# Kernel optimization log

Hardware: AMD Instinct MI355X
Metric: run time of the kernel (lower is better)

## Reference

```python
import jax, jax.numpy as jnp
import numpy as np
from jax import lax

DIM = 192
HEADS = 8
HID = int(DIM * 4.0)

def setup_inputs() -> dict:
    key = jax.random.key(0)
    ks = jax.random.split(key, 10)
    b, c, h, w = 4, DIM, 256, DIM  # w must equal dim for the Mlp over last axis
    x = jax.random.normal(ks[0], (b, c, h, w), dtype=jnp.float32)
    return {
        "x": x,
        "ln1_w": jnp.ones((DIM,), jnp.float32),
        "ln1_b": jnp.zeros((DIM,), jnp.float32),
        "temperature": jnp.ones((HEADS, 1, 1), jnp.float32),
        "qkv_w": jax.random.normal(ks[1], (3 * DIM, DIM), jnp.float32) * 0.02,
        "dw_w": jax.random.normal(ks[2], (3 * DIM, 1, 3, 3), jnp.float32) * 0.1,
        "proj_w": jax.random.normal(ks[3], (DIM, DIM), jnp.float32) * 0.02,
        "ln2_w": jnp.ones((DIM,), jnp.float32),
        "ln2_b": jnp.zeros((DIM,), jnp.float32),
        "fc1_w": jax.random.normal(ks[4], (HID, DIM), jnp.float32) * 0.02,
        "fc1_b": jnp.zeros((HID,), jnp.float32),
        "fc2_w": jax.random.normal(ks[5], (DIM, HID), jnp.float32) * 0.02,
        "fc2_b": jnp.zeros((DIM,), jnp.float32),
    }

def _layernorm_chan(x, w, b):
    # WithBias LayerNorm over the channel axis, per spatial location (to_3d -> LN -> to_4d)
    mu = jnp.mean(x, axis=1, keepdims=True)
    var = jnp.mean((x - mu) ** 2, axis=1, keepdims=True)
    y = (x - mu) / jnp.sqrt(var + 1e-5)
    return y * w[None, :, None, None] + b[None, :, None, None]

def _l2norm(x, axis=-1, eps=1e-12):
    n = jnp.sqrt(jnp.sum(x * x, axis=axis, keepdims=True))
    return x / jnp.maximum(n, eps)

def _attention(x, temperature, qkv_w, dw_w, proj_w):
    b, c, h, w = x.shape
    # 1x1 conv (pointwise GEMM) then 3x3 depthwise conv
    qkv = jnp.einsum('oc,bchw->bohw', qkv_w, x)
    qkv = lax.conv_general_dilated(qkv, dw_w, window_strides=(1, 1), padding='SAME',
                                   feature_group_count=3 * c,
                                   dimension_numbers=('NCHW', 'OIHW', 'NCHW'))
    q, k, v = jnp.split(qkv, 3, axis=1)
    ch = c // HEADS
    q = q.reshape(b, HEADS, ch, h * w)
    k = k.reshape(b, HEADS, ch, h * w)
    v = v.reshape(b, HEADS, ch, h * w)
    q = _l2norm(q)
    k = _l2norm(k)
    attn = jnp.einsum('bhcn,bhdn->bhcd', q, k) * temperature  # [b,H,ch,ch] channel attention
    attn = jax.nn.softmax(attn, axis=-1)
    out = jnp.einsum('bhcd,bhdn->bhcn', attn, v).reshape(b, c, h, w)
    return jnp.einsum('oc,bchw->bohw', proj_w, out)

def _mlp(x, fc1_w, fc1_b, fc2_w, fc2_b):
    # nn.Linear applied on the LAST axis (w == dim), matching the original quirk
    h1 = jnp.einsum('bchw,ow->bcho', x, fc1_w) + fc1_b
    h1 = jax.nn.gelu(h1, approximate=False)
    return jnp.einsum('bcho,do->bchd', h1, fc2_w) + fc2_b

def reference(x, ln1_w, ln1_b, temperature, qkv_w, dw_w, proj_w, ln2_w, ln2_b, fc1_w, fc1_b, fc2_w, fc2_b):
    x = x + _attention(_layernorm_chan(x, ln1_w, ln1_b), temperature, qkv_w, dw_w, proj_w)
    x = x + _mlp(_layernorm_chan(x, ln2_w, ln2_b), fc1_w, fc1_b, fc2_w, fc2_b)
    return x
```

## Files before the change

### kernel.cpp

```cpp
#include <hip/hip_runtime.h>
#include <math.h>

#define SSP   49152
#define HDIM  256
#define WDIM  192
#define CDIM  192
#define NHEAD 8
#define CH    24
#define OC3   576
#define HIDF  768
#define NB    4
#define SCCH  24

typedef short bf16x8 __attribute__((ext_vector_type(8)));
typedef short bf16x4 __attribute__((ext_vector_type(4)));
typedef float f32x4  __attribute__((ext_vector_type(4)));

__device__ inline short f2bf(float f) {
  unsigned u = __float_as_uint(f);
  u += 0x7fffu + ((u >> 16) & 1u);
  return (short)(u >> 16);
}
__device__ inline float bf2f(short h) {
  return __uint_as_float(((unsigned)(unsigned short)h) << 16);
}

__device__ inline void gl_lds16(const short* g, short* l) {
  __builtin_amdgcn_global_load_lds(
      (const __attribute__((address_space(1))) unsigned int*)g,
      (__attribute__((address_space(3))) unsigned int*)l, 16, 0, 0);
}

__global__ __launch_bounds__(256) void cvt_all(const float* __restrict__ s0,
                                               const float* __restrict__ s1,
                                               const float* __restrict__ s2,
                                               const float* __restrict__ s3,
                                               short* __restrict__ dst) {
  int i = blockIdx.x * 256 + threadIdx.x;
  float v;
  if (i < 110592)      v = s0[i];
  else if (i < 147456) v = s1[i - 110592];
  else if (i < 294912) v = s2[i - 147456];
  else                 v = s3[i - 294912];
  dst[i] = f2bf(v);
}

template <bool TRANS>
__global__ __launch_bounds__(256) void ln_bf16(const float* __restrict__ x,
                                               const float* __restrict__ w,
                                               const float* __restrict__ bia,
                                               short* __restrict__ outp) {
  __shared__ float xs[192][68];
  __shared__ float ps[4][64], pq[4][64], mus[64], rst[64];
  const int tid = threadIdx.x;
  const int s0 = blockIdx.x * 64;
  const float* xb = x + (size_t)blockIdx.y * CDIM * SSP;
  short* outb = outp + (size_t)blockIdx.y * CDIM * SSP;
#pragma unroll
  for (int it = 0; it < 12; ++it) {
    int u = it * 256 + tid;
    int c = u >> 4, q = u & 15;
    float4 v = *(const float4*)(xb + (size_t)c * SSP + s0 + q * 4);
    *(float4*)&xs[c][q * 4] = v;
  }
  __syncthreads();
  {
    int s = tid & 63, p = tid >> 6;
    float sm = 0.f, sq = 0.f;
    for (int c = p * 48; c < p * 48 + 48; ++c) {
      float v = xs[c][s]; sm += v; sq += v * v;
    }
    ps[p][s] = sm; pq[p][s] = sq;
  }
  __syncthreads();
  if (tid < 64) {
    float sm = ps[0][tid] + ps[1][tid] + ps[2][tid] + ps[3][tid];
    float sq = pq[0][tid] + pq[1][tid] + pq[2][tid] + pq[3][tid];
    float mu = sm * (1.f / CDIM);
    mus[tid] = mu;
    rst[tid] = rsqrtf(sq * (1.f / CDIM) - mu * mu + 1e-5f);
  }
  __syncthreads();
  if (TRANS) {
#pragma unroll
    for (int it = 0; it < 6; ++it) {
      int u = it * 256 + tid;
      int c8 = u >> 6, sr = u & 63;
      float mu = mus[sr], r = rst[sr];
      bf16x8 o;
#pragma unroll
      for (int j = 0; j < 8; ++j) {
        int c = c8 * 8 + j;
        o[j] = f2bf((xs[c][sr] - mu) * r * w[c] + bia[c]);
      }
      *(bf16x8*)(outb + (size_t)(s0 + sr) * CDIM + c8 * 8) = o;
    }
  } else {
#pragma unroll
    for (int it = 0; it < 6; ++it) {
      int u = it * 256 + tid;
      int c = u >> 3, sv = u & 7;
      float wc = w[c], bc = bia[c];
      bf16x8 o;
#pragma unroll
      for (int j = 0; j < 8; ++j) {
        int s = sv * 8 + j;
        o[j] = f2bf((xs[c][s] - mus[s]) * rst[s] * wc + bc);
      }
      *(bf16x8*)(outb + (size_t)c * SSP + s0 + sv * 8) = o;
    }
  }
}

template <bool RESID, bool OUT_BF16>
__global__ __launch_bounds__(256) void mfma_gemm(
    const short* __restrict__ A, const short* __restrict__ B,
    const float* __restrict__ resid, void* __restrict__ Cv,
    int M, int N, int K, long long strideB, long long strideC) {
  __shared__ short As[2][64 * 32];
  __shared__ short Bs[2][256 * 32];
  const int tid = threadIdx.x;
  const int m0 = blockIdx.y * 64, n0 = blockIdx.x * 256;
  const long long z = blockIdx.z;
  const short* Bz = B + z * strideB;
  const int w = tid >> 6, lane = tid & 63;
  const int r16 = lane & 15, kg = lane >> 4;
  const int arow = tid >> 2, ac4 = tid & 3;

  f32x4 acc[4][4] = {};

  for (int k0 = 0; k0 < K; k0 += 64) {
#pragma unroll
    for (int s = 0; s < 2; ++s) {
      gl_lds16(A + (size_t)(m0 + arow) * K + k0 + s * 32 + ac4 * 8, As[s] + w * 512);
#pragma unroll
      for (int p = 0; p < 4; ++p) {
        int flat = p * 256 + tid;
        int brow = flat >> 2, bc4 = flat & 3;
        gl_lds16(Bz + (size_t)(n0 + brow) * K + k0 + s * 32 + bc4 * 8, Bs[s] + p * 2048 + w * 512);
      }
    }
    __syncthreads();
#pragma unroll
    for (int s = 0; s < 2; ++s) {
      bf16x8 af[4], bfr[4];
#pragma unroll
      for (int i = 0; i < 4; ++i)
        af[i] = *(bf16x8*)(&As[s][(i * 16 + r16) * 32 + kg * 8]);
#pragma unroll
      for (int j = 0; j < 4; ++j)
        bfr[j] = *(bf16x8*)(&Bs[s][(w * 64 + j * 16 + r16) * 32 + kg * 8]);
#pragma unroll
      for (int i = 0; i < 4; ++i)
#pragma unroll
        for (int j = 0; j < 4; ++j)
          acc[i][j] = __builtin_amdgcn_mfma_f32_16x16x32_bf16(af[i], bfr[j], acc[i][j], 0, 0, 0);
    }
    __syncthreads();
  }

  float* Cf = (float*)Cv + z * strideC;
  short* Ch = (short*)Cv + z * strideC;
  const float* R = RESID ? resid + z * strideC : nullptr;
#pragma unroll
  for (int i = 0; i < 4; ++i) {
#pragma unroll
    for (int j = 0; j < 4; ++j) {
#pragma unroll
      for (int t = 0; t < 4; ++t) {
        int m = m0 + i * 16 + kg * 4 + t;
        int n = n0 + w * 64 + j * 16 + r16;
        float v = acc[i][j][t];
        size_t idx = (size_t)m * N + n;
        if (RESID) v += R[idx];
        if (OUT_BF16) Ch[idx] = f2bf(v); else Cf[idx] = v;
      }
    }
  }
}

__global__ __launch_bounds__(256) void dwconv_tile(const short* __restrict__ in,
                                                   const float* __restrict__ w9,
                                                   short* __restrict__ out) {
  __shared__ short tile[34][208];
  const int tid = threadIdx.x;
  const int ch = blockIdx.x >> 3;
  const int slab = blockIdx.x & 7;
  const int o = ch % OC3;
  const int y0 = slab * 32;
  float wr[9];
#pragma unroll
  for (int i = 0; i < 9; ++i) wr[i] = w9[o * 9 + i];
  const short* ip = in + (size_t)ch * SSP;

  if (tid < 34) { tile[tid][7] = 0; tile[tid][200] = 0; }
#pragma unroll
  for (int i = 0; i < 4; ++i) {
    int idx = i * 256 + tid;
    if (idx < 816) {
      int row = idx / 24, cx = idx - row * 24;
      int gy = y0 + row - 1;
      bf16x8 v = {};
      if (gy >= 0 && gy < HDIM) v = *(const bf16x8*)(ip + gy * WDIM + cx * 8);
      *(bf16x8*)(&tile[row][8 + cx * 8]) = v;
    }
  }
  __syncthreads();

  short* op = out + (size_t)ch * SSP;
#pragma unroll
  for (int g = 0; g < 3; ++g) {
    int G = g * 256 + tid;
    int r = G / 24, cx = G - (G / 24) * 24;
    int cb = cx * 8 + 7;
    float a[10], b[10], c[10];
#pragma unroll
    for (int d = 0; d < 10; ++d) {
      a[d] = bf2f(tile[r][cb + d]);
      b[d] = bf2f(tile[r + 1][cb + d]);
      c[d] = bf2f(tile[r + 2][cb + d]);
    }
    bf16x8 ov;
#pragma unroll
    for (int j = 0; j < 8; ++j) {
      float acc = wr[0] * a[j] + wr[1] * a[j + 1] + wr[2] * a[j + 2]
                + wr[3] * b[j] + wr[4] * b[j + 1] + wr[5] * b[j + 2]
                + wr[6] * c[j] + wr[7] * c[j + 1] + wr[8] * c[j + 2];
      ov[j] = f2bf(acc);
    }
    *(bf16x8*)(op + (y0 + r) * WDIM + cx * 8) = ov;
  }
}

__global__ __launch_bounds__(256) void scores_stage1(const short* __restrict__ D,
                                                     float* __restrict__ pdot,
                                                     float* __restrict__ qss,
                                                     float* __restrict__ kss) {
  int ch = blockIdx.x, h = blockIdx.y, b = blockIdx.z;
  __shared__ float qs[24][260];
  __shared__ float ks[24][260];
  int tid = threadIdx.x;
  int w = tid >> 6, lane = tid & 63;
  int c0 = w * 6;
  float acc[6] = {0.f, 0.f, 0.f, 0.f, 0.f, 0.f};
  float ssacc = 0.f;
  const short* qb = D + ((size_t)b * OC3 + h * CH) * SSP;
  const short* kb = D + ((size_t)b * OC3 + CDIM + h * CH) * SSP;
  for (int it = 0; it < 8; ++it) {
    int s0 = ch * 2048 + it * 256;
#pragma unroll
    for (int p = 0; p < 3; ++p) {
      int u = p * 256 + tid;
      int row = u >> 5, col8 = u & 31;
      bf16x8 qv = *(const bf16x8*)(qb + (size_t)row * SSP + s0 + col8 * 8);
      bf16x8 kv = *(const bf16x8*)(kb + (size_t)row * SSP + s0 + col8 * 8);
#pragma unroll
      for (int j = 0; j < 8; ++j) {
        qs[row][col8 * 8 + j] = bf2f(qv[j]);
        ks[row][col8 * 8 + j] = bf2f(kv[j]);
      }
    }
    __syncthreads();
    if (w < 2 && lane < 24) {
      const float (*src)[260] = (w == 0) ? qs : ks;
      for (int s = 0; s < 256; s += 4) {
        float4 v = *(const float4*)&src[lane][s];
        ssacc += v.x * v.x + v.y * v.y + v.z * v.z + v.w * v.w;
      }
    }
    if (lane < 24) {
      for (int s = 0; s < 256; s += 4) {
        float4 kv = *(float4*)&ks[lane][s];
#pragma unroll
        for (int i = 0; i < 6; ++i) {
          float4 qv = *(float4*)&qs[c0 + i][s];
          acc[i] += qv.x * kv.x + qv.y * kv.y + qv.z * kv.z + qv.w * kv.w;
        }
      }
    }
    __syncthreads();
  }
  if (lane < 24) {
    float* pb = pdot + (size_t)b * (NHEAD * CH * CH * SCCH);
#pragma unroll
    for (int i = 0; i < 6; ++i)
      pb[(((size_t)h * CH + (c0 + i)) * CH + lane) * SCCH + ch] = acc[i];
    if (w == 0) qss[(((size_t)b * NHEAD + h) * CH + lane) * SCCH + ch] = ssacc;
    if (w == 1) kss[(((size_t)b * NHEAD + h) * CH + lane) * SCCH + ch] = ssacc;
  }
}

__global__ void scores_reduce(const float* __restrict__ pdot,
                              const float* __restrict__ qss,
                              const float* __restrict__ kss,
                              const float* __restrict__ temp,
                              float* __restrict__ atn) {
  int c = blockIdx.x, h = blockIdx.y, b = blockIdx.z;
  int tid = threadIdx.x;
  __shared__ float row[24];
  if (tid < 24) {
    const float* p = pdot + (size_t)b * (NHEAD * CH * CH * SCCH) +
                     (((size_t)h * CH + c) * CH + tid) * SCCH;
    float s = 0.f;
#pragma unroll
    for (int i = 0; i < SCCH; ++i) s += p[i];
    const float* pq = qss + (((size_t)b * NHEAD + h) * CH + c) * SCCH;
    const float* pk = kss + (((size_t)b * NHEAD + h) * CH + tid) * SCCH;
    float sq = 0.f, sk = 0.f;
#pragma unroll
    for (int i = 0; i < SCCH; ++i) { sq += pq[i]; sk += pk[i]; }
    float rq = 1.f / fmaxf(sqrtf(sq), 1e-12f);
    float rk = 1.f / fmaxf(sqrtf(sk), 1e-12f);
    row[tid] = s * rq * rk * temp[h];
  }
  __syncthreads();
  if (tid < 24) {
    float mx = -1e30f;
    for (int d = 0; d < 24; ++d) mx = fmaxf(mx, row[d]);
    float sum = 0.f;
    for (int d = 0; d < 24; ++d) sum += expf(row[d] - mx);
    atn[((size_t)b * NHEAD + h) * 576 + c * CH + tid] = expf(row[tid] - mx) / sum;
  }
}

__global__ __launch_bounds__(256) void attn_pv_bf16(const short* __restrict__ D,
                                                    const float* __restrict__ atn,
                                                    short* __restrict__ pvt) {
  int nb = blockIdx.x, h = blockIdx.y, b = blockIdx.z;
  __shared__ float aL[24][24];
  int tid = threadIdx.x;
  const float* ab = atn + ((size_t)b * NHEAD + h) * 576;
  for (int i = tid; i < 576; i += 256) aL[i / 24][i % 24] = ab[i];
  __syncthreads();
  int n = nb * 256 + tid;
  const short* vb = D + ((size_t)b * OC3 + 2 * CDIM + h * CH) * SSP + n;
  float vv[24];
#pragma unroll
  for (int d = 0; d < 24; ++d) vv[d] = bf2f(vb[(size_t)d * SSP]);
  short* ob = pvt + (size_t)b * SSP * CDIM + (size_t)n * CDIM + h * CH;
  bf16x8 o0, o1, o2;
#pragma unroll
  for (int cc = 0; cc < 24; ++cc) {
    float s = 0.f;
#pragma unroll
    for (int d = 0; d < 24; ++d) s += aL[cc][d] * vv[d];
    short bv = f2bf(s);
    if (cc < 8) o0[cc & 7] = bv; else if (cc < 16) o1[cc & 7] = bv; else o2[cc & 7] = bv;
  }
  *(bf16x8*)(ob) = o0;
  *(bf16x8*)(ob + 8) = o1;
  *(bf16x8*)(ob + 16) = o2;
}

__global__ __launch_bounds__(512, 4) void mlp_fused(const short* __restrict__ y2,
                                                    const short* __restrict__ w1,
                                                    const short* __restrict__ w2,
                                                    const float* __restrict__ b1,
                                                    const float* __restrict__ b2,
                                                    float* __restrict__ out) {
  __shared__ short w1s[64 * 200];
  __shared__ short w2s[192 * 72];
  __shared__ short h1s[128 * 72];
  const int tid = threadIdx.x;
  const int m0 = blockIdx.x * 128;
  const int w = tid >> 6, lane = tid & 63;
  const int r16 = lane & 15, kg = lane >> 4;
  const int wm = w >> 1, wn = w & 1;

  const int u0 = tid, u1 = 512 + tid, u2 = 1024 + tid;
  const int s1r[3] = {u0 / 24, u1 / 24, u2 / 24};
  const int s1c[3] = {u0 % 24, u1 % 24, u2 % 24};
  const int s2r[3] = {u0 / 8, u1 / 8, u2 / 8};
  const int s2c[3] = {u0 % 8, u1 % 8, u2 % 8};

  bf16x8 afr[2][6];
#pragma unroll
  for (int ks = 0; ks < 6; ++ks)
#pragma unroll
    for (int i = 0; i < 2; ++i)
      afr[i][ks] = *(const bf16x8*)(y2 + (size_t)(m0 + wm * 32 + i * 16 + r16) * CDIM + ks * 32 + kg * 8);

  f32x4 bacc[2][6] = {};

  for (int hc = 0; hc < 12; ++hc) {
#pragma unroll
    for (int it = 0; it < 3; ++it) {
      *(bf16x8*)(&w1s[s1r[it] * 200 + s1c[it] * 8]) =
          *(const bf16x8*)(w1 + (size_t)(hc * 64 + s1r[it]) * CDIM + s1c[it] * 8);
      *(bf16x8*)(&w2s[s2r[it] * 72 + s2c[it] * 8]) =
          *(const bf16x8*)(w2 + (size_t)s2r[it] * HIDF + hc * 64 + s2c[it] * 8);
    }
    __syncthreads();

    f32x4 pacc[2][2] = {};
#pragma unroll
    for (int ks = 0; ks < 6; ++ks) {
      bf16x8 bg[2];
#pragma unroll
      for (int j = 0; j < 2; ++j)
        bg[j] = *(bf16x8*)(&w1s[(wn * 32 + j * 16 + r16) * 200 + ks * 32 + kg * 8]);
#pragma unroll
      for (int i = 0; i < 2; ++i)
#pragma unroll
        for (int j = 0; j < 2; ++j)
          pacc[i][j] = __builtin_amdgcn_mfma_f32_16x16x32_bf16(bg[j], afr[i][ks], pacc[i][j], 0, 0, 0);
    }
#pragma unroll
    for (int i = 0; i < 2; ++i) {
      int mr = wm * 32 + i * 16 + r16;
#pragma unroll
      for (int j = 0; j < 2; ++j) {
        int hid0 = wn * 32 + j * 16 + kg * 4;
        bf16x4 pk;
#pragma unroll
        for (int t = 0; t < 4; ++t) {
          float v = pacc[i][j][t] + b1[hc * 64 + hid0 + t];
          v = 0.5f * v * (1.f + erff(v * 0.70710678118654752f));
          pk[t] = f2bf(v);
        }
        *(bf16x4*)(&h1s[mr * 72 + hid0]) = pk;
      }
    }
    __syncthreads();

#pragma unroll
    for (int ks = 0; ks < 2; ++ks) {
      bf16x8 a2[2];
#pragma unroll
      for (int i = 0; i < 2; ++i)
        a2[i] = *(bf16x8*)(&h1s[(wm * 32 + i * 16 + r16) * 72 + ks * 32 + kg * 8]);
#pragma unroll
      for (int j = 0; j < 6; ++j) {
        bf16x8 b2g = *(bf16x8*)(&w2s[(wn * 96 + j * 16 + r16) * 72 + ks * 32 + kg * 8]);
#pragma unroll
        for (int i = 0; i < 2; ++i)
          bacc[i][j] = __builtin_amdgcn_mfma_f32_16x16x32_bf16(a2[i], b2g, bacc[i][j], 0, 0, 0);
      }
    }
    __syncthreads();
  }

#pragma unroll
  for (int i = 0; i < 2; ++i)
#pragma unroll
    for (int j = 0; j < 6; ++j)
#pragma unroll
      for (int t = 0; t < 4; ++t) {
        int m = m0 + wm * 32 + i * 16 + kg * 4 + t;
        int n = wn * 96 + j * 16 + r16;
        size_t idx = (size_t)m * CDIM + n;
        out[idx] = bacc[i][j][t] + b2[n] + out[idx];
      }
}

extern "C" void kernel_launch(void* const* d_in, const int* in_sizes, int n_in,
                              void* d_out, int out_size, void* d_ws, size_t ws_size,
                              hipStream_t stream) {
  const float* x      = (const float*)d_in[0];
  const float* ln1_w  = (const float*)d_in[1];
  const float* ln1_b  = (const float*)d_in[2];
  const float* temp   = (const float*)d_in[3];
  const float* qkv_w  = (const float*)d_in[4];
  const float* dw_w   = (const float*)d_in[5];
  const float* proj_w = (const float*)d_in[6];
  const float* ln2_w  = (const float*)d_in[7];
  const float* ln2_b  = (const float*)d_in[8];
  const float* fc1_w  = (const float*)d_in[9];
  const float* fc1_b  = (const float*)d_in[10];
  const float* fc2_w  = (const float*)d_in[11];
  const float* fc2_b  = (const float*)d_in[12];
  float* out = (float*)d_out;

  char* base = (char*)d_ws;
  short* wq  = (short*)base;
  short* wp  = wq + 110592;
  short* w1  = wp + 36864;
  short* w2  = w1 + 147456;
  float* pdot= (float*)(base + 890880);
  float* qss = (float*)(base + 2660352);
  float* kss = (float*)(base + 2734080);
  float* atn = (float*)(base + 2807808);
  short* Dv  = (short*)(base + 4194304);
  short* y1t = Dv;
  short* T   = (short*)(base + 230686720);
  short* pvt = T;
  short* y2  = (short*)(base + 457179136);

  cvt_all<<<dim3(1728), 256, 0, stream>>>(qkv_w, proj_w, fc1_w, fc2_w, wq);

  ln_bf16<true><<<dim3(SSP / 64, NB), 256, 0, stream>>>(x, ln1_w, ln1_b, y1t);
  mfma_gemm<false, true><<<dim3(SSP / 256, OC3 / 64, NB), 256, 0, stream>>>(
      wq, y1t, nullptr, T, OC3, SSP, CDIM, (long long)SSP * CDIM, (long long)OC3 * SSP);
  dwconv_tile<<<dim3(NB * OC3 * 8), 256, 0, stream>>>(T, dw_w, Dv);
  scores_stage1<<<dim3(SCCH, NHEAD, NB), 256, 0, stream>>>(Dv, pdot, qss, kss);
  scores_reduce<<<dim3(CH, NHEAD, NB), 64, 0, stream>>>(pdot, qss, kss, temp, atn);
  attn_pv_bf16<<<dim3(SSP / 256, NHEAD, NB), 256, 0, stream>>>(Dv, atn, pvt);
  mfma_gemm<true, false><<<dim3(SSP / 256, CDIM / 64, NB), 256, 0, stream>>>(
      wp, pvt, x, out, CDIM, SSP, CDIM, (long long)SSP * CDIM, (long long)CDIM * SSP);
  ln_bf16<false><<<dim3(SSP / 64, NB), 256, 0, stream>>>(out, ln2_w, ln2_b, y2);
  mlp_fused<<<dim3(196608 / 128), 512, 0, stream>>>(y2, w1, w2, fc1_b, fc2_b, out);
}
```

Baseline: 1.019 ms.

## Split fused MLP into two generic MFMA GEMMs with bias/GELU epilogues

Replaces the single fused MLP kernel, which kept the hidden activation in LDS, with two launches of a generalized MFMA GEMM template that takes a configurable N tile and optional bias, GELU and residual epilogues. The first GEMM writes the GELU'd hidden activation in bf16 to a workspace buffer. The second GEMM reads it back and adds bias and the residual. This trades extra global memory traffic for the hidden tensor against what may be a more efficient GEMM tiling, with more parallelism and less per-block synchronization than the fused kernel.

```diff
diff --git a/kernel.cpp b/kernel.cpp
--- a/kernel.cpp
+++ b/kernel.cpp
@@ -11,6 +11,7 @@
 #define HIDF  768
 #define NB    4
 #define SCCH  24
+#define MROWS 196608
 
 typedef short bf16x8 __attribute__((ext_vector_type(8)));
 typedef short bf16x4 __attribute__((ext_vector_type(4)));
@@ -112,29 +113,32 @@
   }
 }
 
-template <bool RESID, bool OUT_BF16>
-__global__ __launch_bounds__(256) void mfma_gemm(
+template <int BN, bool BIAS, bool GELU, bool RESID, bool OUT_BF16>
+__global__ __launch_bounds__(256) void mfma_gemmx(
     const short* __restrict__ A, const short* __restrict__ B,
-    const float* __restrict__ resid, void* __restrict__ Cv,
-    int M, int N, int K, long long strideB, long long strideC) {
+    const float* __restrict__ bias, const float* __restrict__ resid,
+    void* __restrict__ Cv, int M, int N, int K,
+    long long strideB, long long strideC) {
+  constexpr int FN = BN / 64;
+  constexpr int WCOL = BN / 4;
   __shared__ short As[2][64 * 32];
-  __shared__ short Bs[2][256 * 32];
+  __shared__ short Bs[2][BN * 32];
   const int tid = threadIdx.x;
-  const int m0 = blockIdx.y * 64, n0 = blockIdx.x * 256;
+  const int m0 = blockIdx.y * 64, n0 = blockIdx.x * BN;
   const long long z = blockIdx.z;
   const short* Bz = B + z * strideB;
   const int w = tid >> 6, lane = tid & 63;
   const int r16 = lane & 15, kg = lane >> 4;
   const int arow = tid >> 2, ac4 = tid & 3;
 
-  f32x4 acc[4][4] = {};
+  f32x4 acc[4][FN] = {};
 
   for (int k0 = 0; k0 < K; k0 += 64) {
 #pragma unroll
     for (int s = 0; s < 2; ++s) {
       gl_lds16(A + (size_t)(m0 + arow) * K + k0 + s * 32 + ac4 * 8, As[s] + w * 512);
 #pragma unroll
-      for (int p = 0; p < 4; ++p) {
+      for (int p = 0; p < FN; ++p) {
         int flat = p * 256 + tid;
         int brow = flat >> 2, bc4 = flat & 3;
         gl_lds16(Bz + (size_t)(n0 + brow) * K + k0 + s * 32 + bc4 * 8, Bs[s] + p * 2048 + w * 512);
@@ -143,17 +147,17 @@
     __syncthreads();
 #pragma unroll
     for (int s = 0; s < 2; ++s) {
-      bf16x8 af[4], bfr[4];
+      bf16x8 af[4], bfr[FN];
 #pragma unroll
       for (int i = 0; i < 4; ++i)
         af[i] = *(bf16x8*)(&As[s][(i * 16 + r16) * 32 + kg * 8]);
 #pragma unroll
-      for (int j = 0; j < 4; ++j)
-        bfr[j] = *(bf16x8*)(&Bs[s][(w * 64 + j * 16 + r16) * 32 + kg * 8]);
+      for (int j = 0; j < FN; ++j)
+        bfr[j] = *(bf16x8*)(&Bs[s][(w * WCOL + j * 16 + r16) * 32 + kg * 8]);
 #pragma unroll
       for (int i = 0; i < 4; ++i)
 #pragma unroll
-        for (int j = 0; j < 4; ++j)
+        for (int j = 0; j < FN; ++j)
           acc[i][j] = __builtin_amdgcn_mfma_f32_16x16x32_bf16(af[i], bfr[j], acc[i][j], 0, 0, 0);
     }
     __syncthreads();
@@ -165,12 +169,14 @@
 #pragma unroll
   for (int i = 0; i < 4; ++i) {
 #pragma unroll
-    for (int j = 0; j < 4; ++j) {
+    for (int j = 0; j < FN; ++j) {
 #pragma unroll
       for (int t = 0; t < 4; ++t) {
         int m = m0 + i * 16 + kg * 4 + t;
-        int n = n0 + w * 64 + j * 16 + r16;
+        int n = n0 + w * WCOL + j * 16 + r16;
         float v = acc[i][j][t];
+        if (BIAS) v += bias[n];
+        if (GELU) v = 0.5f * v * (1.f + erff(v * 0.70710678118654752f));
         size_t idx = (size_t)m * N + n;
         if (RESID) v += R[idx];
         if (OUT_BF16) Ch[idx] = f2bf(v); else Cf[idx] = v;
@@ -350,107 +356,6 @@
   *(bf16x8*)(ob) = o0;
   *(bf16x8*)(ob + 8) = o1;
   *(bf16x8*)(ob + 16) = o2;
-}
-
-__global__ __launch_bounds__(512, 4) void mlp_fused(const short* __restrict__ y2,
-                                                    const short* __restrict__ w1,
-                                                    const short* __restrict__ w2,
-                                                    const float* __restrict__ b1,
-                                                    const float* __restrict__ b2,
-                                                    float* __restrict__ out) {
-  __shared__ short w1s[64 * 200];
-  __shared__ short w2s[192 * 72];
-  __shared__ short h1s[128 * 72];
-  const int tid = threadIdx.x;
-  const int m0 = blockIdx.x * 128;
-  const int w = tid >> 6, lane = tid & 63;
-  const int r16 = lane & 15, kg = lane >> 4;
-  const int wm = w >> 1, wn = w & 1;
-
-  const int u0 = tid, u1 = 512 + tid, u2 = 1024 + tid;
-  const int s1r[3] = {u0 / 24, u1 / 24, u2 / 24};
-  const int s1c[3] = {u0 % 24, u1 % 24, u2 % 24};
-  const int s2r[3] = {u0 / 8, u1 / 8, u2 / 8};
-  const int s2c[3] = {u0 % 8, u1 % 8, u2 % 8};
-
-  bf16x8 afr[2][6];
-#pragma unroll
-  for (int ks = 0; ks < 6; ++ks)
-#pragma unroll
-    for (int i = 0; i < 2; ++i)
-      afr[i][ks] = *(const bf16x8*)(y2 + (size_t)(m0 + wm * 32 + i * 16 + r16) * CDIM + ks * 32 + kg * 8);
-
-  f32x4 bacc[2][6] = {};
-
-  for (int hc = 0; hc < 12; ++hc) {
-#pragma unroll
-    for (int it = 0; it < 3; ++it) {
-      *(bf16x8*)(&w1s[s1r[it] * 200 + s1c[it] * 8]) =
-          *(const bf16x8*)(w1 + (size_t)(hc * 64 + s1r[it]) * CDIM + s1c[it] * 8);
-      *(bf16x8*)(&w2s[s2r[it] * 72 + s2c[it] * 8]) =
-          *(const bf16x8*)(w2 + (size_t)s2r[it] * HIDF + hc * 64 + s2c[it] * 8);
-    }
-    __syncthreads();
-
-    f32x4 pacc[2][2] = {};
-#pragma unroll
-    for (int ks = 0; ks < 6; ++ks) {
-      bf16x8 bg[2];
-#pragma unroll
-      for (int j = 0; j < 2; ++j)
-        bg[j] = *(bf16x8*)(&w1s[(wn * 32 + j * 16 + r16) * 200 + ks * 32 + kg * 8]);
-#pragma unroll
-      for (int i = 0; i < 2; ++i)
-#pragma unroll
-        for (int j = 0; j < 2; ++j)
-          pacc[i][j] = __builtin_amdgcn_mfma_f32_16x16x32_bf16(bg[j], afr[i][ks], pacc[i][j], 0, 0, 0);
-    }
-#pragma unroll
-    for (int i = 0; i < 2; ++i) {
-      int mr = wm * 32 + i * 16 + r16;
-#pragma unroll
-      for (int j = 0; j < 2; ++j) {
-        int hid0 = wn * 32 + j * 16 + kg * 4;
-        bf16x4 pk;
-#pragma unroll
-        for (int t = 0; t < 4; ++t) {
-          float v = pacc[i][j][t] + b1[hc * 64 + hid0 + t];
-          v = 0.5f * v * (1.f + erff(v * 0.70710678118654752f));
-          pk[t] = f2bf(v);
-        }
-        *(bf16x4*)(&h1s[mr * 72 + hid0]) = pk;
-      }
-    }
-    __syncthreads();
-
-#pragma unroll
-    for (int ks = 0; ks < 2; ++ks) {
-      bf16x8 a2[2];
-#pragma unroll
-      for (int i = 0; i < 2; ++i)
-        a2[i] = *(bf16x8*)(&h1s[(wm * 32 + i * 16 + r16) * 72 + ks * 32 + kg * 8]);
-#pragma unroll
-      for (int j = 0; j < 6; ++j) {
-        bf16x8 b2g = *(bf16x8*)(&w2s[(wn * 96 + j * 16 + r16) * 72 + ks * 32 + kg * 8]);
-#pragma unroll
-        for (int i = 0; i < 2; ++i)
-          bacc[i][j] = __builtin_amdgcn_mfma_f32_16x16x32_bf16(a2[i], b2g, bacc[i][j], 0, 0, 0);
-      }
-    }
-    __syncthreads();
-  }
-
-#pragma unroll
-  for (int i = 0; i < 2; ++i)
-#pragma unroll
-    for (int j = 0; j < 6; ++j)
-#pragma unroll
-      for (int t = 0; t < 4; ++t) {
-        int m = m0 + wm * 32 + i * 16 + kg * 4 + t;
-        int n = wn * 96 + j * 16 + r16;
-        size_t idx = (size_t)m * CDIM + n;
-        out[idx] = bacc[i][j][t] + b2[n] + out[idx];
-      }
 }
 
 extern "C" void kernel_launch(void* const* d_in, const int* in_sizes, int n_in,
@@ -482,6 +387,7 @@
   float* atn = (float*)(base + 2807808);
   short* Dv  = (short*)(base + 4194304);
   short* y1t = Dv;
+  short* h1  = Dv;
   short* T   = (short*)(base + 230686720);
   short* pvt = T;
   short* y2  = (short*)(base + 457179136);
@@ -489,14 +395,17 @@
   cvt_all<<<dim3(1728), 256, 0, stream>>>(qkv_w, proj_w, fc1_w, fc2_w, wq);
 
   ln_bf16<true><<<dim3(SSP / 64, NB), 256, 0, stream>>>(x, ln1_w, ln1_b, y1t);
-  mfma_gemm<false, true><<<dim3(SSP / 256, OC3 / 64, NB), 256, 0, stream>>>(
-      wq, y1t, nullptr, T, OC3, SSP, CDIM, (long long)SSP * CDIM, (long long)OC3 * SSP);
+  mfma_gemmx<256, false, false, false, true><<<dim3(SSP / 256, OC3 / 64, NB), 256, 0, stream>>>(
+      wq, y1t, nullptr, nullptr, T, OC3, SSP, CDIM, (long long)SSP * CDIM, (long long)OC3 * SSP);
   dwconv_tile<<<dim3(NB * OC3 * 8), 256, 0, stream>>>(T, dw_w, Dv);
   scores_stage1<<<dim3(SCCH, NHEAD, NB), 256, 0, stream>>>(Dv, pdot, qss, kss);
   scores_reduce<<<dim3(CH, NHEAD, NB), 64, 0, stream>>>(pdot, qss, kss, temp, atn);
   attn_pv_bf16<<<dim3(SSP / 256, NHEAD, NB), 256, 0, stream>>>(Dv, atn, pvt);
-  mfma_gemm<true, false><<<dim3(SSP / 256, CDIM / 64, NB), 256, 0, stream>>>(
-      wp, pvt, x, out, CDIM, SSP, CDIM, (long long)SSP * CDIM, (long long)CDIM * SSP);
+  mfma_gemmx<256, false, false, true, false><<<dim3(SSP / 256, CDIM / 64, NB), 256, 0, stream>>>(
+      wp, pvt, nullptr, x, out, CDIM, SSP, CDIM, (long long)SSP * CDIM, (long long)CDIM * SSP);
   ln_bf16<false><<<dim3(SSP / 64, NB), 256, 0, stream>>>(out, ln2_w, ln2_b, y2);
-  mlp_fused<<<dim3(196608 / 128), 512, 0, stream>>>(y2, w1, w2, fc1_b, fc2_b, out);
-}
+  mfma_gemmx<256, true, true, false, true><<<dim3(HIDF / 256, MROWS / 64, 1), 256, 0, stream>>>(
+      y2, w1, fc1_b, nullptr, h1, MROWS, HIDF, CDIM, 0LL, 0LL);
+  mfma_gemmx<192, true, false, true, false><<<dim3(1, MROWS / 64, 1), 256, 0, stream>>>(
+      h1, w2, fc2_b, out, out, MROWS, CDIM, HIDF, 0LL, 0LL);
+}
```

After: 1.010 ms. No clear change (-0.9%).

## Store intermediate residual in bf16 and prefetch MLP weights via registers

Applied to the files above, without the earlier changes.

The attention projection now writes the first residual sum as bf16 into a workspace buffer instead of fp32 into the output. The second LayerNorm and the MLP epilogue read that bf16 buffer, which roughly halves the traffic on that intermediate tensor. mlp_fused now stages the y2 tile in shared memory rather than holding it in registers, and prefetches the next weight chunk into registers while computing the current one. The launch-bounds occupancy hint is removed, and the larger shared-memory footprint and bf16 rounding of the residual may cut occupancy and accuracy.

```diff
diff --git a/kernel.cpp b/kernel.cpp
--- a/kernel.cpp
+++ b/kernel.cpp
@@ -45,8 +45,8 @@
   dst[i] = f2bf(v);
 }
 
-template <bool TRANS>
-__global__ __launch_bounds__(256) void ln_bf16(const float* __restrict__ x,
+template <bool TRANS, bool INBF16>
+__global__ __launch_bounds__(256) void ln_bf16(const void* __restrict__ xin,
                                                const float* __restrict__ w,
                                                const float* __restrict__ bia,
                                                short* __restrict__ outp) {
@@ -54,14 +54,26 @@
   __shared__ float ps[4][64], pq[4][64], mus[64], rst[64];
   const int tid = threadIdx.x;
   const int s0 = blockIdx.x * 64;
-  const float* xb = x + (size_t)blockIdx.y * CDIM * SSP;
   short* outb = outp + (size_t)blockIdx.y * CDIM * SSP;
-#pragma unroll
-  for (int it = 0; it < 12; ++it) {
-    int u = it * 256 + tid;
-    int c = u >> 4, q = u & 15;
-    float4 v = *(const float4*)(xb + (size_t)c * SSP + s0 + q * 4);
-    *(float4*)&xs[c][q * 4] = v;
+  if (INBF16) {
+    const short* xb = (const short*)xin + (size_t)blockIdx.y * CDIM * SSP;
+#pragma unroll
+    for (int it = 0; it < 6; ++it) {
+      int u = it * 256 + tid;
+      int c = u >> 3, q = u & 7;
+      bf16x8 v = *(const bf16x8*)(xb + (size_t)c * SSP + s0 + q * 8);
+#pragma unroll
+      for (int j = 0; j < 8; ++j) xs[c][q * 8 + j] = bf2f(v[j]);
+    }
+  } else {
+    const float* xb = (const float*)xin + (size_t)blockIdx.y * CDIM * SSP;
+#pragma unroll
+    for (int it = 0; it < 12; ++it) {
+      int u = it * 256 + tid;
+      int c = u >> 4, q = u & 15;
+      float4 v = *(const float4*)(xb + (size_t)c * SSP + s0 + q * 4);
+      *(float4*)&xs[c][q * 4] = v;
+    }
   }
   __syncthreads();
   {
@@ -113,7 +125,7 @@
 }
 
 template <bool RESID, bool OUT_BF16>
-__global__ __launch_bounds__(256) void mfma_gemm(
+__global__ __launch_bounds__(256) void mfma_gemmx(
     const short* __restrict__ A, const short* __restrict__ B,
     const float* __restrict__ resid, void* __restrict__ Cv,
     int M, int N, int K, long long strideB, long long strideC) {
@@ -352,12 +364,14 @@
   *(bf16x8*)(ob + 16) = o2;
 }
 
-__global__ __launch_bounds__(512, 4) void mlp_fused(const short* __restrict__ y2,
-                                                    const short* __restrict__ w1,
-                                                    const short* __restrict__ w2,
-                                                    const float* __restrict__ b1,
-                                                    const float* __restrict__ b2,
-                                                    float* __restrict__ out) {
+__global__ __launch_bounds__(512) void mlp_fused(const short* __restrict__ y2,
+                                                 const short* __restrict__ w1,
+                                                 const short* __restrict__ w2,
+                                                 const float* __restrict__ b1,
+                                                 const float* __restrict__ b2,
+                                                 const short* __restrict__ x1w,
+                                                 float* __restrict__ out) {
+  __shared__ short y2s[128 * 200];
   __shared__ short w1s[64 * 200];
   __shared__ short w2s[192 * 72];
   __shared__ short h1s[128 * 72];
@@ -373,29 +387,40 @@
   const int s2r[3] = {u0 / 8, u1 / 8, u2 / 8};
   const int s2c[3] = {u0 % 8, u1 % 8, u2 % 8};
 
-  bf16x8 afr[2][6];
-#pragma unroll
-  for (int ks = 0; ks < 6; ++ks)
-#pragma unroll
-    for (int i = 0; i < 2; ++i)
-      afr[i][ks] = *(const bf16x8*)(y2 + (size_t)(m0 + wm * 32 + i * 16 + r16) * CDIM + ks * 32 + kg * 8);
+#pragma unroll
+  for (int it = 0; it < 6; ++it) {
+    int u = it * 512 + tid;
+    int row = u / 24, cx = u % 24;
+    *(bf16x8*)(&y2s[row * 200 + cx * 8]) =
+        *(const bf16x8*)(y2 + (size_t)(m0 + row) * CDIM + cx * 8);
+  }
+#pragma unroll
+  for (int it = 0; it < 3; ++it) {
+    *(bf16x8*)(&w1s[s1r[it] * 200 + s1c[it] * 8]) =
+        *(const bf16x8*)(w1 + (size_t)s1r[it] * CDIM + s1c[it] * 8);
+    *(bf16x8*)(&w2s[s2r[it] * 72 + s2c[it] * 8]) =
+        *(const bf16x8*)(w2 + (size_t)s2r[it] * HIDF + s2c[it] * 8);
+  }
+  __syncthreads();
 
   f32x4 bacc[2][6] = {};
+  bf16x8 rw1[3], rw2[3];
 
   for (int hc = 0; hc < 12; ++hc) {
-#pragma unroll
-    for (int it = 0; it < 3; ++it) {
-      *(bf16x8*)(&w1s[s1r[it] * 200 + s1c[it] * 8]) =
-          *(const bf16x8*)(w1 + (size_t)(hc * 64 + s1r[it]) * CDIM + s1c[it] * 8);
-      *(bf16x8*)(&w2s[s2r[it] * 72 + s2c[it] * 8]) =
-          *(const bf16x8*)(w2 + (size_t)s2r[it] * HIDF + hc * 64 + s2c[it] * 8);
-    }
-    __syncthreads();
-
+    if (hc < 11) {
+#pragma unroll
+      for (int it = 0; it < 3; ++it) {
+        rw1[it] = *(const bf16x8*)(w1 + (size_t)((hc + 1) * 64 + s1r[it]) * CDIM + s1c[it] * 8);
+        rw2[it] = *(const bf16x8*)(w2 + (size_t)s2r[it] * HIDF + (hc + 1) * 64 + s2c[it] * 8);
+      }
+    }
     f32x4 pacc[2][2] = {};
 #pragma unroll
     for (int ks = 0; ks < 6; ++ks) {
-      bf16x8 bg[2];
+      bf16x8 af[2], bg[2];
+#pragma unroll
+      for (int i = 0; i < 2; ++i)
+        af[i] = *(bf16x8*)(&y2s[(wm * 32 + i * 16 + r16) * 200 + ks * 32 + kg * 8]);
 #pragma unroll
       for (int j = 0; j < 2; ++j)
         bg[j] = *(bf16x8*)(&w1s[(wn * 32 + j * 16 + r16) * 200 + ks * 32 + kg * 8]);
@@ -403,7 +428,7 @@
       for (int i = 0; i < 2; ++i)
 #pragma unroll
         for (int j = 0; j < 2; ++j)
-          pacc[i][j] = __builtin_amdgcn_mfma_f32_16x16x32_bf16(bg[j], afr[i][ks], pacc[i][j], 0, 0, 0);
+          pacc[i][j] = __builtin_amdgcn_mfma_f32_16x16x32_bf16(bg[j], af[i], pacc[i][j], 0, 0, 0);
     }
 #pragma unroll
     for (int i = 0; i < 2; ++i) {
@@ -438,6 +463,15 @@
       }
     }
     __syncthreads();
+
+    if (hc < 11) {
+#pragma unroll
+      for (int it = 0; it < 3; ++it) {
+        *(bf16x8*)(&w1s[s1r[it] * 200 + s1c[it] * 8]) = rw1[it];
+        *(bf16x8*)(&w2s[s2r[it] * 72 + s2c[it] * 8]) = rw2[it];
+      }
+      __syncthreads();
+    }
   }
 
 #pragma unroll
@@ -449,7 +483,7 @@
         int m = m0 + wm * 32 + i * 16 + kg * 4 + t;
         int n = wn * 96 + j * 16 + r16;
         size_t idx = (size_t)m * CDIM + n;
-        out[idx] = bacc[i][j][t] + b2[n] + out[idx];
+        out[idx] = bacc[i][j][t] + b2[n] + bf2f(x1w[idx]);
       }
 }
 
@@ -482,21 +516,22 @@
   float* atn = (float*)(base + 2807808);
   short* Dv  = (short*)(base + 4194304);
   short* y1t = Dv;
+  short* x1w = Dv;
   short* T   = (short*)(base + 230686720);
   short* pvt = T;
   short* y2  = (short*)(base + 457179136);
 
   cvt_all<<<dim3(1728), 256, 0, stream>>>(qkv_w, proj_w, fc1_w, fc2_w, wq);
 
-  ln_bf16<true><<<dim3(SSP / 64, NB), 256, 0, stream>>>(x, ln1_w, ln1_b, y1t);
-  mfma_gemm<false, true><<<dim3(SSP / 256, OC3 / 64, NB), 256, 0, stream>>>(
+  ln_bf16<true, false><<<dim3(SSP / 64, NB), 256, 0, stream>>>(x, ln1_w, ln1_b, y1t);
+  mfma_gemmx<false, true><<<dim3(SSP / 256, OC3 / 64, NB), 256, 0, stream>>>(
       wq, y1t, nullptr, T, OC3, SSP, CDIM, (long long)SSP * CDIM, (long long)OC3 * SSP);
   dwconv_tile<<<dim3(NB * OC3 * 8), 256, 0, stream>>>(T, dw_w, Dv);
   scores_stage1<<<dim3(SCCH, NHEAD, NB), 256, 0, stream>>>(Dv, pdot, qss, kss);
   scores_reduce<<<dim3(CH, NHEAD, NB), 64, 0, stream>>>(pdot, qss, kss, temp, atn);
   attn_pv_bf16<<<dim3(SSP / 256, NHEAD, NB), 256, 0, stream>>>(Dv, atn, pvt);
-  mfma_gemm<true, false><<<dim3(SSP / 256, CDIM / 64, NB), 256, 0, stream>>>(
-      wp, pvt, x, out, CDIM, SSP, CDIM, (long long)SSP * CDIM, (long long)CDIM * SSP);
-  ln_bf16<false><<<dim3(SSP / 64, NB), 256, 0, stream>>>(out, ln2_w, ln2_b, y2);
-  mlp_fused<<<dim3(196608 / 128), 512, 0, stream>>>(y2, w1, w2, fc1_b, fc2_b, out);
-}
+  mfma_gemmx<true, true><<<dim3(SSP / 256, CDIM / 64, NB), 256, 0, stream>>>(
+      wp, pvt, x, x1w, CDIM, SSP, CDIM, (long long)SSP * CDIM, (long long)CDIM * SSP);
+  ln_bf16<false, true><<<dim3(SSP / 64, NB), 256, 0, stream>>>(x1w, ln2_w, ln2_b, y2);
+  mlp_fused<<<dim3(196608 / 128), 512, 0, stream>>>(y2, w1, w2, fc1_b, fc2_b, x1w, out);
+}
```

Result: faster. 914.6 us (-10.3%).
